# Performance work log

Measured on AMD Instinct MI355X. Metric: run time of the kernel, lower is better.

Reference implementation:

```python
import jax, jax.numpy as jnp
import numpy as np

N_NODES = 100000
N_EDGES = 1600000
FEAT = 64
HID = 128
HEADS = 4
OUT = 128
EPS_BN = 1e-5


def _gat_layer(h_in, src, dst, W, a_src, a_dst, bias, heads, out_c, concat, n_nodes):
    # h: [N, H, C]
    h = (h_in @ W).reshape(n_nodes, heads, out_c)
    alpha_src = jnp.sum(h * a_src, axis=-1)  # [N, H]
    alpha_dst = jnp.sum(h * a_dst, axis=-1)  # [N, H]
    e = jax.nn.leaky_relu(alpha_src[src] + alpha_dst[dst], negative_slope=0.2)  # [E, H]
    # segment softmax over incoming edges of each dst node
    e_max = jax.ops.segment_max(e, dst, num_segments=n_nodes)  # [N, H]
    ex = jnp.exp(e - e_max[dst])
    denom = jax.ops.segment_sum(ex, dst, num_segments=n_nodes)  # [N, H]
    alpha = ex / denom[dst]  # [E, H]
    # weighted scatter-aggregate of source features
    out = jax.ops.segment_sum(h[src] * alpha[:, :, None], dst, num_segments=n_nodes)  # [N, H, C]
    if concat:
        out = out.reshape(n_nodes, heads * out_c)
    else:
        out = out.mean(axis=1)
    return out + bias


def setup_inputs() -> dict:
    key = jax.random.key(0)
    ks = jax.random.split(key, 12)
    s = 0.1
    x = jax.random.normal(ks[0], (N_NODES, FEAT), dtype=jnp.float32)
    edge_index = jax.random.randint(ks[1], (2, N_EDGES), 0, N_NODES, dtype=jnp.int64)
    C1 = HID // HEADS
    return {
        "x": x,
        "edge_index": edge_index,
        "Wp": jax.random.normal(ks[2], (FEAT, HID), jnp.float32) * s,
        "bp": jnp.zeros((HID,), jnp.float32),
        "W1": jax.random.normal(ks[3], (HID, HEADS * C1), jnp.float32) * s,
        "att_src1": jax.random.normal(ks[4], (HEADS, C1), jnp.float32) * s,
        "att_dst1": jax.random.normal(ks[5], (HEADS, C1), jnp.float32) * s,
        "b1": jnp.zeros((HID,), jnp.float32),
        "gamma": jnp.ones((HID,), jnp.float32),
        "beta": jnp.zeros((HID,), jnp.float32),
        "W2": jax.random.normal(ks[6], (HID, HEADS * OUT), jnp.float32) * s,
        "att_src2": jax.random.normal(ks[7], (HEADS, OUT), jnp.float32) * s,
        "att_dst2": jax.random.normal(ks[8], (HEADS, OUT), jnp.float32) * s,
        "b2": jnp.zeros((OUT,), jnp.float32),
        "Wo": jax.random.normal(ks[9], (OUT, OUT), jnp.float32) * s,
        "bo": jnp.zeros((OUT,), jnp.float32),
    }


def reference(x, edge_index, Wp, bp, W1, att_src1, att_dst1, b1, gamma, beta,
              W2, att_src2, att_dst2, b2, Wo, bo):
    n = x.shape[0]
    # add self-loops (PyG GATConv default)
    loop = jnp.arange(n, dtype=edge_index.dtype)
    src = jnp.concatenate([edge_index[0], loop])
    dst = jnp.concatenate([edge_index[1], loop])

    h = jax.nn.relu(x @ Wp + bp)  # node_proj + relu

    # layer 1: concat heads -> HID
    h = _gat_layer(h, src, dst, W1, att_src1, att_dst1, b1, HEADS, HID // HEADS, True, n)
    # BatchNorm1d eval (fresh running stats: mean=0, var=1) + ELU (dropout off in eval)
    h = h * (gamma / jnp.sqrt(1.0 + EPS_BN)) + beta
    h = jax.nn.elu(h)

    # layer 2: average heads -> OUT
    h = _gat_layer(h, src, dst, W2, att_src2, att_dst2, b2, HEADS, OUT, False, n)

    # batch=None path: mean over all nodes
    g = h.mean(axis=0, keepdims=True)  # [1, OUT]
    return jax.nn.relu(g @ Wo + bo)
```

## Files before the change

### kernel.cpp

```cpp
#include <hip/hip_runtime.h>

#define N_N 100000
#define N_E 1600000
#define E_T (N_E + N_N)

#define NBKT 196
#define BKT_CAP 12288
#define CHUNK 4096
#define EPT 16

typedef long long ll;
typedef unsigned int uint;
typedef unsigned short ushort;
typedef unsigned char uchar;
typedef float floatx2 __attribute__((ext_vector_type(2)));

__device__ __forceinline__ float lrelu(float v){ return v > 0.f ? v : 0.2f*v; }

__device__ __forceinline__ uint pk_fp8_quad(float a, float b, float c, float d){
  int w = __builtin_amdgcn_cvt_pk_fp8_f32(a, b, 0, false);
  w = __builtin_amdgcn_cvt_pk_fp8_f32(c, d, w, true);
  return (uint)w;
}
__device__ __forceinline__ floatx2 unpk_fp8(uint v, int wsel){
  floatx2 lo = __builtin_amdgcn_cvt_pk_f32_fp8((int)v, false);
  floatx2 hi = __builtin_amdgcn_cvt_pk_f32_fp8((int)v, true);
  return wsel ? hi : lo;
}

__global__ void k_detect(const int* __restrict__ ei32, int* __restrict__ mode) {
  int m = 1;
  for (int i = 1; i < 16; i += 2) if (ei32[i] != 0) m = 0;
  *mode = m;
}

__device__ __forceinline__ void load_edge(const void* eiv, int mode, int e, int& s, int& d) {
  if (e < N_E) {
    if (mode) {
      const ll* p = (const ll*)eiv;
      s = (int)p[e]; d = (int)p[N_E + e];
    } else {
      const int* p = (const int*)eiv;
      s = p[e]; d = p[N_E + e];
    }
  } else { s = d = e - N_E; }
}

__global__ void k_zeroi(int* __restrict__ p, int n) {
  for (int i = blockIdx.x*blockDim.x + threadIdx.x; i < n; i += gridDim.x*blockDim.x)
    p[i] = 0;
}

__global__ __launch_bounds__(256) void k_bucket_blk(const void* __restrict__ eiv,
    const int* __restrict__ modep, int* __restrict__ bktpos, uint* __restrict__ stage)
{
  __shared__ int cnt[NBKT], base[NBKT], lrank[NBKT];
  int m = *modep;
  int t = threadIdx.x;
  int e0 = blockIdx.x * CHUNK;
  int nedge = E_T - e0; if (nedge > CHUNK) nedge = CHUNK;
  for (int i = t; i < NBKT; i += 256) { cnt[i] = 0; lrank[i] = 0; }
  __syncthreads();
  uint pk[EPT]; int bb[EPT];
  #pragma unroll
  for (int i = 0; i < EPT; ++i) {
    int idx = t + i*256;
    if (idx < nedge) {
      int e = e0 + idx, s, d;
      load_edge(eiv, m, e, s, d);
      bb[i] = d >> 9;
      pk[i] = ((uint)(d & 511) << 17) | (uint)s;
      atomicAdd(&cnt[bb[i]], 1);
    } else bb[i] = -1;
  }
  __syncthreads();
  for (int i = t; i < NBKT; i += 256)
    if (cnt[i] > 0) base[i] = atomicAdd(&bktpos[i*16], cnt[i]);
  __syncthreads();
  #pragma unroll
  for (int i = 0; i < EPT; ++i) {
    if (bb[i] >= 0) {
      int b = bb[i];
      int r = atomicAdd(&lrank[b], 1);
      int off = base[b] + r;
      if (off < BKT_CAP) stage[(size_t)b*BKT_CAP + off] = pk[i];
    }
  }
}

__global__ void k_bktscan(const int* __restrict__ bktpos, int* __restrict__ bktbase,
    int* __restrict__ rptrN)
{
  if (threadIdx.x == 0) {
    int run = 0;
    for (int b = 0; b < NBKT; ++b) { bktbase[b] = run; run += bktpos[b*16]; }
    *rptrN = run;
  }
}

__global__ __launch_bounds__(256) void k_bucket2(const int* __restrict__ bktpos,
    const int* __restrict__ bktbase, const uint* __restrict__ stage,
    int* __restrict__ csr_col, int* __restrict__ rptr)
{
  __shared__ int cntA[512], pA[512], pB[512], lpos[512];
  int b = blockIdx.x, t = threadIdx.x;
  int cnt = bktpos[b*16];
  if (cnt > BKT_CAP) cnt = BKT_CAP;
  int base = bktbase[b];
  const uint* st = stage + (size_t)b*BKT_CAP;
  for (int i = t; i < 512; i += 256) { cntA[i] = 0; lpos[i] = 0; }
  __syncthreads();
  for (int i = t; i < cnt; i += 256) atomicAdd(&cntA[st[i] >> 17], 1);
  __syncthreads();
  int* src = pA; int* dst = pB;
  for (int i = t; i < 512; i += 256) pA[i] = cntA[i];
  __syncthreads();
  for (int off = 1; off < 512; off <<= 1) {
    for (int i = t; i < 512; i += 256) {
      int v = src[i]; if (i >= off) v += src[i - off]; dst[i] = v;
    }
    __syncthreads();
    int* tmp = src; src = dst; dst = tmp;
  }
  int nb0 = b*512;
  for (int i = t; i < 512; i += 256) {
    int node = nb0 + i;
    if (node < N_N) rptr[node] = base + src[i] - cntA[i];
  }
  __syncthreads();
  for (int i = t; i < cnt; i += 256) {
    uint pk = st[i];
    int dlow = (int)(pk >> 17), s = (int)(pk & 0x1FFFFu);
    int r = atomicAdd(&lpos[dlow], 1);
    csr_col[base + (src[dlow] - cntA[dlow]) + r] = s;
  }
}

__global__ __launch_bounds__(256) void k_fused12(const float* __restrict__ x,
    const float* __restrict__ Wp, const float* __restrict__ bp,
    const float* __restrict__ W1, const float* __restrict__ avs,
    const float* __restrict__ avd, uchar* __restrict__ Hb8,
    float* __restrict__ as_o, float* __restrict__ ad_o)
{
  __shared__ float wl[64*128];
  __shared__ float h0s[32*132];
  __shared__ float xr[32*68];
  const int t = threadIdx.x;
  const int r0g = blockIdx.x * 32;
  const int tx = t & 31, ty = t >> 5;
  const int c0 = tx*4, r0 = ty*4;
  for (int i = t; i < 64*128; i += 256) wl[i] = Wp[i];
  for (int i = t; i < 32*64; i += 256) {
    int r = i >> 6, k = i & 63;
    xr[r*68 + k] = x[(size_t)(r0g + r)*64 + k];
  }
  __syncthreads();
  {
    float acc[4][4] = {};
    for (int k = 0; k < 64; ++k) {
      float4 wv = *(const float4*)&wl[k*128 + c0];
      float x0 = xr[(r0+0)*68+k], x1 = xr[(r0+1)*68+k];
      float x2 = xr[(r0+2)*68+k], x3 = xr[(r0+3)*68+k];
      acc[0][0] += x0*wv.x; acc[0][1] += x0*wv.y; acc[0][2] += x0*wv.z; acc[0][3] += x0*wv.w;
      acc[1][0] += x1*wv.x; acc[1][1] += x1*wv.y; acc[1][2] += x1*wv.z; acc[1][3] += x1*wv.w;
      acc[2][0] += x2*wv.x; acc[2][1] += x2*wv.y; acc[2][2] += x2*wv.z; acc[2][3] += x2*wv.w;
      acc[3][0] += x3*wv.x; acc[3][1] += x3*wv.y; acc[3][2] += x3*wv.z; acc[3][3] += x3*wv.w;
    }
    float4 bb = *(const float4*)&bp[c0];
    for (int i = 0; i < 4; ++i) {
      h0s[(r0+i)*132 + c0    ] = fmaxf(acc[i][0] + bb.x, 0.f);
      h0s[(r0+i)*132 + c0 + 1] = fmaxf(acc[i][1] + bb.y, 0.f);
      h0s[(r0+i)*132 + c0 + 2] = fmaxf(acc[i][2] + bb.z, 0.f);
      h0s[(r0+i)*132 + c0 + 3] = fmaxf(acc[i][3] + bb.w, 0.f);
    }
  }
  float acc[4][4] = {};
  for (int kc = 0; kc < 2; ++kc) {
    const int k0 = kc*64;
    __syncthreads();
    for (int i = t; i < 64*128; i += 256) wl[i] = W1[k0*128 + i];
    __syncthreads();
    for (int k = 0; k < 64; ++k) {
      float4 wv = *(const float4*)&wl[k*128 + c0];
      int kk = k0 + k;
      float x0 = h0s[(r0+0)*132+kk], x1 = h0s[(r0+1)*132+kk];
      float x2 = h0s[(r0+2)*132+kk], x3 = h0s[(r0+3)*132+kk];
      acc[0][0] += x0*wv.x; acc[0][1] += x0*wv.y; acc[0][2] += x0*wv.z; acc[0][3] += x0*wv.w;
      acc[1][0] += x1*wv.x; acc[1][1] += x1*wv.y; acc[1][2] += x1*wv.z; acc[1][3] += x1*wv.w;
      acc[2][0] += x2*wv.x; acc[2][1] += x2*wv.y; acc[2][2] += x2*wv.z; acc[2][3] += x2*wv.w;
      acc[3][0] += x3*wv.x; acc[3][1] += x3*wv.y; acc[3][2] += x3*wv.z; acc[3][3] += x3*wv.w;
    }
  }
  for (int i = 0; i < 4; ++i) {
    int r = r0g + r0 + i;
    ((uint*)&Hb8[(size_t)r*128])[tx] =
      pk_fp8_quad(acc[i][0], acc[i][1], acc[i][2], acc[i][3]);
  }
  float4 sa = *(const float4*)&avs[c0];
  float4 da = *(const float4*)&avd[c0];
  for (int i = 0; i < 4; ++i) {
    float vs = acc[i][0]*sa.x + acc[i][1]*sa.y + acc[i][2]*sa.z + acc[i][3]*sa.w;
    float vd = acc[i][0]*da.x + acc[i][1]*da.y + acc[i][2]*da.z + acc[i][3]*da.w;
    vs += __shfl_xor(vs, 1); vs += __shfl_xor(vs, 2); vs += __shfl_xor(vs, 4);
    vd += __shfl_xor(vd, 1); vd += __shfl_xor(vd, 2); vd += __shfl_xor(vd, 4);
    if ((tx & 7) == 0) {
      int r = r0g + r0 + i;
      as_o[r*4 + (tx >> 3)] = vs;
      ad_o[r*4 + (tx >> 3)] = vd;
    }
  }
}

__global__ void k_fold2(const float* __restrict__ W2,
    const float* __restrict__ att_s2, const float* __restrict__ att_d2,
    float* __restrict__ vs2, float* __restrict__ vd2)
{
  int t = threadIdx.x;
  int k = t & 127, hh = t >> 7;
  float accs = 0.f, accd = 0.f;
  for (int c = 0; c < 128; ++c) {
    float w = W2[(size_t)k*512 + hh*128 + c];
    accs += w * att_s2[hh*128 + c];
    accd += w * att_d2[hh*128 + c];
  }
  vs2[hh*128 + k] = accs;
  vd2[hh*128 + k] = accd;
}

__global__ __launch_bounds__(256) void k_agg1(const int* __restrict__ rptr,
    const int* __restrict__ csr_col, const uchar* __restrict__ Hb8,
    const float* __restrict__ as1, const float* __restrict__ ad1,
    const float* __restrict__ b1, const float* __restrict__ gamma,
    const float* __restrict__ beta, const float* __restrict__ vs2,
    const float* __restrict__ vd2, uchar* __restrict__ a1f8,
    float* __restrict__ as2, float* __restrict__ ad2)
{
  int wid = threadIdx.x >> 6, l = threadIdx.x & 63;
  int n = blockIdx.x*4 + wid;
  if (n >= N_N) return;
  int jm = l & 15, hm = l >> 4;
  const int wsel = l & 1, widx = l >> 1;
  const int wsrc = l & 48;
  float adm = ad1[n*4 + hm];
  int beg = rptr[n], end = rptr[n+1];
  float accx = 0.f, accy = 0.f, den = 0.f;
  for (int e0 = beg; e0 < end; e0 += 16) {
    int ne = end - e0; if (ne > 16) ne = 16;
    int sM = 0; float wM = 0.f;
    if (jm < ne) {
      sM = csr_col[e0 + jm];
      wM = __expf(lrelu(as1[sM*4 + hm] + adm));
    }
    den += wM;
    int j = 0;
    for (; j + 4 <= ne; j += 4) {
      int s0 = __shfl(sM, j),   s1 = __shfl(sM, j+1);
      int s2 = __shfl(sM, j+2), s3 = __shfl(sM, j+3);
      uint h0 = ((const uint*)&Hb8[(size_t)s0*128])[widx];
      uint h1 = ((const uint*)&Hb8[(size_t)s1*128])[widx];
      uint h2 = ((const uint*)&Hb8[(size_t)s2*128])[widx];
      uint h3 = ((const uint*)&Hb8[(size_t)s3*128])[widx];
      float w0 = __shfl(wM, wsrc + j),   w1 = __shfl(wM, wsrc + j+1);
      float w2 = __shfl(wM, wsrc + j+2), w3 = __shfl(wM, wsrc + j+3);
      floatx2 v0 = unpk_fp8(h0, wsel), v1 = unpk_fp8(h1, wsel);
      floatx2 v2 = unpk_fp8(h2, wsel), v3 = unpk_fp8(h3, wsel);
      accx += w0*v0.x + w1*v1.x + w2*v2.x + w3*v3.x;
      accy += w0*v0.y + w1*v1.y + w2*v2.y + w3*v3.y;
    }
    for (; j < ne; ++j) {
      int s = __shfl(sM, j);
      float w = __shfl(wM, wsrc + j);
      uint hv = ((const uint*)&Hb8[(size_t)s*128])[widx];
      floatx2 dv = unpk_fp8(hv, wsel);
      accx += w * dv.x;
      accy += w * dv.y;
    }
  }
  den += __shfl_xor(den, 1); den += __shfl_xor(den, 2);
  den += __shfl_xor(den, 4); den += __shfl_xor(den, 8);
  float inv = 1.f / den;
  int c = 2*l;
  const float sc = 0.9999950000374997f;
  float vx = (accx*inv + b1[c])   * (gamma[c]   * sc) + beta[c];
  float vy = (accy*inv + b1[c+1]) * (gamma[c+1] * sc) + beta[c+1];
  vx = vx > 0.f ? vx : __expf(vx) - 1.f;
  vy = vy > 0.f ? vy : __expf(vy) - 1.f;
  int pk = __builtin_amdgcn_cvt_pk_fp8_f32(vx, vy, 0, false);
  *(ushort*)&a1f8[(size_t)n*128 + c] = (ushort)pk;
  #pragma unroll
  for (int hh = 0; hh < 4; ++hh) {
    float2 wsv = *(const float2*)&vs2[hh*128 + c];
    float2 wdv = *(const float2*)&vd2[hh*128 + c];
    float ps = wsv.x*vx + wsv.y*vy;
    float pd = wdv.x*vx + wdv.y*vy;
    ps += __shfl_xor(ps, 1); ps += __shfl_xor(ps, 2); ps += __shfl_xor(ps, 4);
    ps += __shfl_xor(ps, 8); ps += __shfl_xor(ps, 16); ps += __shfl_xor(ps, 32);
    pd += __shfl_xor(pd, 1); pd += __shfl_xor(pd, 2); pd += __shfl_xor(pd, 4);
    pd += __shfl_xor(pd, 8); pd += __shfl_xor(pd, 16); pd += __shfl_xor(pd, 32);
    if (l == 0) { as2[n*4 + hh] = ps; ad2[n*4 + hh] = pd; }
  }
}

__global__ __launch_bounds__(512) void k_tail2(const int* __restrict__ rptr,
    const int* __restrict__ csr_col, const uchar* __restrict__ a1f8,
    const float* __restrict__ as2, const float* __restrict__ ad2,
    float* __restrict__ u)
{
  int wid = threadIdx.x >> 6, l = threadIdx.x & 63;
  int jm = l & 15, hm = l >> 4;
  int c0 = jm * 8;
  const int wsrc = l & 48;
  float acc[8] = {};
  for (int n = blockIdx.x*8 + wid; n < N_N; n += gridDim.x*8) {
    int beg = rptr[n], end = rptr[n+1];
    float adm = ad2[n*4 + hm];
    float accn[8] = {};
    float dsum = 0.f;
    for (int e0 = beg; e0 < end; e0 += 16) {
      int ne = end - e0; if (ne > 16) ne = 16;
      int sM = 0; float wM = 0.f;
      if (jm < ne) {
        sM = csr_col[e0 + jm];
        wM = __expf(lrelu(as2[sM*4 + hm] + adm));
      }
      dsum += wM;
      int j = 0;
      for (; j + 2 <= ne; j += 2) {
        int sa = __shfl(sM, j), sb = __shfl(sM, j+1);
        uint2 ha = *(const uint2*)&a1f8[(size_t)sa*128 + c0];
        uint2 hb = *(const uint2*)&a1f8[(size_t)sb*128 + c0];
        float wa = __shfl(wM, wsrc + j), wb = __shfl(wM, wsrc + j+1);
        floatx2 a0 = __builtin_amdgcn_cvt_pk_f32_fp8((int)ha.x, false);
        floatx2 a1 = __builtin_amdgcn_cvt_pk_f32_fp8((int)ha.x, true);
        floatx2 a2 = __builtin_amdgcn_cvt_pk_f32_fp8((int)ha.y, false);
        floatx2 a3 = __builtin_amdgcn_cvt_pk_f32_fp8((int)ha.y, true);
        floatx2 b0 = __builtin_amdgcn_cvt_pk_f32_fp8((int)hb.x, false);
        floatx2 b1v = __builtin_amdgcn_cvt_pk_f32_fp8((int)hb.x, true);
        floatx2 b2 = __builtin_amdgcn_cvt_pk_f32_fp8((int)hb.y, false);
        floatx2 b3 = __builtin_amdgcn_cvt_pk_f32_fp8((int)hb.y, true);
        accn[0] += wa*a0.x + wb*b0.x; accn[1] += wa*a0.y + wb*b0.y;
        accn[2] += wa*a1.x + wb*b1v.x; accn[3] += wa*a1.y + wb*b1v.y;
        accn[4] += wa*a2.x + wb*b2.x; accn[5] += wa*a2.y + wb*b2.y;
        accn[6] += wa*a3.x + wb*b3.x; accn[7] += wa*a3.y + wb*b3.y;
      }
      for (; j < ne; ++j) {
        int s = __shfl(sM, j);
        float w = __shfl(wM, wsrc + j);
        uint2 hv = *(const uint2*)&a1f8[(size_t)s*128 + c0];
        floatx2 d0 = __builtin_amdgcn_cvt_pk_f32_fp8((int)hv.x, false);
        floatx2 d1 = __builtin_amdgcn_cvt_pk_f32_fp8((int)hv.x, true);
        floatx2 d2 = __builtin_amdgcn_cvt_pk_f32_fp8((int)hv.y, false);
        floatx2 d3 = __builtin_amdgcn_cvt_pk_f32_fp8((int)hv.y, true);
        accn[0] += w * d0.x; accn[1] += w * d0.y;
        accn[2] += w * d1.x; accn[3] += w * d1.y;
        accn[4] += w * d2.x; accn[5] += w * d2.y;
        accn[6] += w * d3.x; accn[7] += w * d3.y;
      }
    }
    dsum += __shfl_xor(dsum, 1); dsum += __shfl_xor(dsum, 2);
    dsum += __shfl_xor(dsum, 4); dsum += __shfl_xor(dsum, 8);
    float inv = 1.f / dsum;
    #pragma unroll
    for (int c = 0; c < 8; ++c) acc[c] += accn[c] * inv;
  }
  __shared__ float us[8][512];
  #pragma unroll
  for (int c = 0; c < 8; ++c) us[wid][hm*128 + c0 + c] = acc[c];
  __syncthreads();
  for (int i = threadIdx.x; i < 512; i += 512) {
    float v = 0.f;
    #pragma unroll
    for (int w = 0; w < 8; ++w) v += us[w][i];
    atomicAdd(&u[i], v);
  }
}

__global__ void k_final2(const float* __restrict__ u, const float* __restrict__ W2,
    const float* __restrict__ b2, const float* __restrict__ Wo,
    const float* __restrict__ bo, float* __restrict__ outp)
{
  __shared__ float g[128];
  int t = threadIdx.x;
  float acc = 0.f;
  for (int h = 0; h < 4; ++h)
    for (int k = 0; k < 128; ++k)
      acc += u[h*128 + k] * W2[(size_t)k*512 + h*128 + t];
  g[t] = acc * (1.f / (4.f * N_N)) + b2[t];
  __syncthreads();
  float o = 0.f;
  for (int c = 0; c < 128; ++c) o += g[c] * Wo[c*128 + t];
  o += bo[t];
  outp[t] = o > 0.f ? o : 0.f;
}

extern "C" void kernel_launch(void* const* d_in, const int* in_sizes, int n_in,
                              void* d_out, int out_size, void* d_ws, size_t ws_size,
                              hipStream_t stream) {
  const float* x    = (const float*)d_in[0];
  const void*  ei   = d_in[1];
  const float* Wp   = (const float*)d_in[2];
  const float* bp   = (const float*)d_in[3];
  const float* W1   = (const float*)d_in[4];
  const float* at_s1= (const float*)d_in[5];
  const float* at_d1= (const float*)d_in[6];
  const float* b1   = (const float*)d_in[7];
  const float* gamma= (const float*)d_in[8];
  const float* beta = (const float*)d_in[9];
  const float* W2   = (const float*)d_in[10];
  const float* at_s2= (const float*)d_in[11];
  const float* at_d2= (const float*)d_in[12];
  const float* b2   = (const float*)d_in[13];
  const float* Wo   = (const float*)d_in[14];
  const float* bo   = (const float*)d_in[15];

  const size_t NN = N_N;
  uchar* hb8   = (uchar*)d_ws;
  uchar* a1f8  = hb8 + NN*128;
  int*   csr_col = (int*)(a1f8 + NN*128);
  int*   rptr    = csr_col + E_T;
  uint*  stage   = (uint*)(rptr + N_N + 1);
  int*   bktpos  = (int*)(stage + (size_t)NBKT*BKT_CAP);
  int*   bktbase = bktpos + NBKT*16;
  float* as1     = (float*)(bktbase + NBKT);
  float* ad1     = as1 + NN*4;
  float* as2     = ad1 + NN*4;
  float* ad2     = as2 + NN*4;
  float* vs2     = ad2 + NN*4;
  float* vd2     = vs2 + 512;
  float* u       = vd2 + 512;
  int*   modep   = (int*)(u + 512);

  size_t required = ((char*)(modep + 1)) - (char*)d_ws;
  if (ws_size < required) return;

  const int NB4 = (N_N + 3) / 4;
  const int NCHUNK = (E_T + CHUNK - 1) / CHUNK;

  k_detect<<<1, 1, 0, stream>>>((const int*)ei, modep);
  k_zeroi<<<16, 256, 0, stream>>>(bktpos, NBKT*16);
  k_zeroi<<<2, 256, 0, stream>>>((int*)u, 512);
  k_bucket_blk<<<NCHUNK, 256, 0, stream>>>(ei, modep, bktpos, stage);
  k_bktscan<<<1, 64, 0, stream>>>(bktpos, bktbase, rptr + N_N);
  k_bucket2<<<NBKT, 256, 0, stream>>>(bktpos, bktbase, stage, csr_col, rptr);

  k_fused12<<<N_N/32, 256, 0, stream>>>(x, Wp, bp, W1, at_s1, at_d1, hb8, as1, ad1);
  k_fold2<<<1, 512, 0, stream>>>(W2, at_s2, at_d2, vs2, vd2);
  k_agg1<<<NB4, 256, 0, stream>>>(rptr, csr_col, hb8, as1, ad1, b1, gamma, beta,
                                  vs2, vd2, a1f8, as2, ad2);

  k_tail2<<<1024, 512, 0, stream>>>(rptr, csr_col, a1f8, as2, ad2, u);
  k_final2<<<1, 128, 0, stream>>>(u, W2, b2, Wo, bo, (float*)d_out);
}
```

Baseline: 387.0 us.

## Merge independent preprocessing kernels into one launch and use packed float2 accumulation

Folds mode detection and the two zeroing kernels into a single init kernel. Merges the edge bucketing, the node projection/layer-1 GEMM and the W2 attention fold into one heterogeneous kernel that dispatches on block index, so these independent stages run concurrently and no longer serialize across launches. The aggregation loops in agg1 and tail2 now accumulate in floatx2 vectors so the compiler can emit packed FMA instructions. Unifying the shared memory footprint may reduce occupancy for the bucketing blocks.

```diff
diff --git a/kernel.cpp b/kernel.cpp
--- a/kernel.cpp
+++ b/kernel.cpp
@@ -8,6 +8,7 @@
 #define BKT_CAP 12288
 #define CHUNK 4096
 #define EPT 16
+#define NPROJ (N_N/32)
 
 typedef long long ll;
 typedef unsigned int uint;
@@ -26,12 +27,6 @@
   floatx2 lo = __builtin_amdgcn_cvt_pk_f32_fp8((int)v, false);
   floatx2 hi = __builtin_amdgcn_cvt_pk_f32_fp8((int)v, true);
   return wsel ? hi : lo;
-}
-
-__global__ void k_detect(const int* __restrict__ ei32, int* __restrict__ mode) {
-  int m = 1;
-  for (int i = 1; i < 16; i += 2) if (ei32[i] != 0) m = 0;
-  *mode = m;
 }
 
 __device__ __forceinline__ void load_edge(const void* eiv, int mode, int e, int& s, int& d) {
@@ -46,45 +41,151 @@
   } else { s = d = e - N_E; }
 }
 
-__global__ void k_zeroi(int* __restrict__ p, int n) {
-  for (int i = blockIdx.x*blockDim.x + threadIdx.x; i < n; i += gridDim.x*blockDim.x)
-    p[i] = 0;
-}
-
-__global__ __launch_bounds__(256) void k_bucket_blk(const void* __restrict__ eiv,
-    const int* __restrict__ modep, int* __restrict__ bktpos, uint* __restrict__ stage)
-{
-  __shared__ int cnt[NBKT], base[NBKT], lrank[NBKT];
-  int m = *modep;
-  int t = threadIdx.x;
-  int e0 = blockIdx.x * CHUNK;
-  int nedge = E_T - e0; if (nedge > CHUNK) nedge = CHUNK;
-  for (int i = t; i < NBKT; i += 256) { cnt[i] = 0; lrank[i] = 0; }
-  __syncthreads();
-  uint pk[EPT]; int bb[EPT];
-  #pragma unroll
-  for (int i = 0; i < EPT; ++i) {
-    int idx = t + i*256;
-    if (idx < nedge) {
-      int e = e0 + idx, s, d;
-      load_edge(eiv, m, e, s, d);
-      bb[i] = d >> 9;
-      pk[i] = ((uint)(d & 511) << 17) | (uint)s;
-      atomicAdd(&cnt[bb[i]], 1);
-    } else bb[i] = -1;
-  }
-  __syncthreads();
-  for (int i = t; i < NBKT; i += 256)
-    if (cnt[i] > 0) base[i] = atomicAdd(&bktpos[i*16], cnt[i]);
-  __syncthreads();
-  #pragma unroll
-  for (int i = 0; i < EPT; ++i) {
-    if (bb[i] >= 0) {
-      int b = bb[i];
-      int r = atomicAdd(&lrank[b], 1);
-      int off = base[b] + r;
-      if (off < BKT_CAP) stage[(size_t)b*BKT_CAP + off] = pk[i];
-    }
+__global__ __launch_bounds__(256) void k_init(const int* __restrict__ ei32,
+    int* __restrict__ bktpos, int* __restrict__ u512, int* __restrict__ mode)
+{
+  int i = blockIdx.x*256 + threadIdx.x;
+  if (i < NBKT*16) bktpos[i] = 0;
+  if (i < 512) u512[i] = 0;
+  if (i == 0) {
+    int m = 1;
+    for (int k = 1; k < 16; k += 2) if (ei32[k] != 0) m = 0;
+    *mode = m;
+  }
+}
+
+__global__ __launch_bounds__(256) void k_mega(
+    const void* __restrict__ eiv, const int* __restrict__ modep,
+    int* __restrict__ bktpos, uint* __restrict__ stage,
+    const float* __restrict__ x, const float* __restrict__ Wp,
+    const float* __restrict__ bp, const float* __restrict__ W1,
+    const float* __restrict__ avs, const float* __restrict__ avd,
+    uchar* __restrict__ Hb8, float* __restrict__ as_o, float* __restrict__ ad_o,
+    const float* __restrict__ W2, const float* __restrict__ att_s2,
+    const float* __restrict__ att_d2, float* __restrict__ vs2, float* __restrict__ vd2)
+{
+  __shared__ float smem[8192 + 4224 + 2176];
+  const int blk = blockIdx.x;
+  const int t = threadIdx.x;
+  const int NCH = (E_T + CHUNK - 1) / CHUNK;
+
+  if (blk < NCH) {
+    int* cnt   = (int*)smem;
+    int* base  = cnt + NBKT;
+    int* lrank = base + NBKT;
+    int m = *modep;
+    int e0 = blk * CHUNK;
+    int nedge = E_T - e0; if (nedge > CHUNK) nedge = CHUNK;
+    for (int i = t; i < NBKT; i += 256) { cnt[i] = 0; lrank[i] = 0; }
+    __syncthreads();
+    uint pk[EPT]; int bb[EPT];
+    #pragma unroll
+    for (int i = 0; i < EPT; ++i) {
+      int idx = t + i*256;
+      if (idx < nedge) {
+        int e = e0 + idx, s, d;
+        load_edge(eiv, m, e, s, d);
+        bb[i] = d >> 9;
+        pk[i] = ((uint)(d & 511) << 17) | (uint)s;
+        atomicAdd(&cnt[bb[i]], 1);
+      } else bb[i] = -1;
+    }
+    __syncthreads();
+    for (int i = t; i < NBKT; i += 256)
+      if (cnt[i] > 0) base[i] = atomicAdd(&bktpos[i*16], cnt[i]);
+    __syncthreads();
+    #pragma unroll
+    for (int i = 0; i < EPT; ++i) {
+      if (bb[i] >= 0) {
+        int b = bb[i];
+        int r = atomicAdd(&lrank[b], 1);
+        int off = base[b] + r;
+        if (off < BKT_CAP) stage[(size_t)b*BKT_CAP + off] = pk[i];
+      }
+    }
+    return;
+  }
+
+  if (blk < NCH + NPROJ) {
+    float* wl  = smem;
+    float* h0s = smem + 8192;
+    float* xr  = smem + 8192 + 4224;
+    const int r0g = (blk - NCH) * 32;
+    const int tx = t & 31, ty = t >> 5;
+    const int c0 = tx*4, r0 = ty*4;
+    for (int i = t; i < 64*128; i += 256) wl[i] = Wp[i];
+    for (int i = t; i < 32*64; i += 256) {
+      int r = i >> 6, k = i & 63;
+      xr[r*68 + k] = x[(size_t)(r0g + r)*64 + k];
+    }
+    __syncthreads();
+    {
+      float acc[4][4] = {};
+      for (int k = 0; k < 64; ++k) {
+        float4 wv = *(const float4*)&wl[k*128 + c0];
+        float x0 = xr[(r0+0)*68+k], x1 = xr[(r0+1)*68+k];
+        float x2 = xr[(r0+2)*68+k], x3 = xr[(r0+3)*68+k];
+        acc[0][0] += x0*wv.x; acc[0][1] += x0*wv.y; acc[0][2] += x0*wv.z; acc[0][3] += x0*wv.w;
+        acc[1][0] += x1*wv.x; acc[1][1] += x1*wv.y; acc[1][2] += x1*wv.z; acc[1][3] += x1*wv.w;
+        acc[2][0] += x2*wv.x; acc[2][1] += x2*wv.y; acc[2][2] += x2*wv.z; acc[2][3] += x2*wv.w;
+        acc[3][0] += x3*wv.x; acc[3][1] += x3*wv.y; acc[3][2] += x3*wv.z; acc[3][3] += x3*wv.w;
+      }
+      float4 bb = *(const float4*)&bp[c0];
+      for (int i = 0; i < 4; ++i) {
+        h0s[(r0+i)*132 + c0    ] = fmaxf(acc[i][0] + bb.x, 0.f);
+        h0s[(r0+i)*132 + c0 + 1] = fmaxf(acc[i][1] + bb.y, 0.f);
+        h0s[(r0+i)*132 + c0 + 2] = fmaxf(acc[i][2] + bb.z, 0.f);
+        h0s[(r0+i)*132 + c0 + 3] = fmaxf(acc[i][3] + bb.w, 0.f);
+      }
+    }
+    float acc[4][4] = {};
+    for (int kc = 0; kc < 2; ++kc) {
+      const int k0 = kc*64;
+      __syncthreads();
+      for (int i = t; i < 64*128; i += 256) wl[i] = W1[k0*128 + i];
+      __syncthreads();
+      for (int k = 0; k < 64; ++k) {
+        float4 wv = *(const float4*)&wl[k*128 + c0];
+        int kk = k0 + k;
+        float x0 = h0s[(r0+0)*132+kk], x1 = h0s[(r0+1)*132+kk];
+        float x2 = h0s[(r0+2)*132+kk], x3 = h0s[(r0+3)*132+kk];
+        acc[0][0] += x0*wv.x; acc[0][1] += x0*wv.y; acc[0][2] += x0*wv.z; acc[0][3] += x0*wv.w;
+        acc[1][0] += x1*wv.x; acc[1][1] += x1*wv.y; acc[1][2] += x1*wv.z; acc[1][3] += x1*wv.w;
+        acc[2][0] += x2*wv.x; acc[2][1] += x2*wv.y; acc[2][2] += x2*wv.z; acc[2][3] += x2*wv.w;
+        acc[3][0] += x3*wv.x; acc[3][1] += x3*wv.y; acc[3][2] += x3*wv.z; acc[3][3] += x3*wv.w;
+      }
+    }
+    for (int i = 0; i < 4; ++i) {
+      int r = r0g + r0 + i;
+      ((uint*)&Hb8[(size_t)r*128])[tx] =
+        pk_fp8_quad(acc[i][0], acc[i][1], acc[i][2], acc[i][3]);
+    }
+    float4 sa = *(const float4*)&avs[c0];
+    float4 da = *(const float4*)&avd[c0];
+    for (int i = 0; i < 4; ++i) {
+      float vs = acc[i][0]*sa.x + acc[i][1]*sa.y + acc[i][2]*sa.z + acc[i][3]*sa.w;
+      float vd = acc[i][0]*da.x + acc[i][1]*da.y + acc[i][2]*da.z + acc[i][3]*da.w;
+      vs += __shfl_xor(vs, 1); vs += __shfl_xor(vs, 2); vs += __shfl_xor(vs, 4);
+      vd += __shfl_xor(vd, 1); vd += __shfl_xor(vd, 2); vd += __shfl_xor(vd, 4);
+      if ((tx & 7) == 0) {
+        int r = r0g + r0 + i;
+        as_o[r*4 + (tx >> 3)] = vs;
+        ad_o[r*4 + (tx >> 3)] = vd;
+      }
+    }
+    return;
+  }
+
+  for (int t2 = t; t2 < 512; t2 += 256) {
+    int k = t2 & 127, hh = t2 >> 7;
+    float accs = 0.f, accd = 0.f;
+    for (int c = 0; c < 128; ++c) {
+      float w = W2[(size_t)k*512 + hh*128 + c];
+      accs += w * att_s2[hh*128 + c];
+      accd += w * att_d2[hh*128 + c];
+    }
+    vs2[hh*128 + k] = accs;
+    vd2[hh*128 + k] = accd;
   }
 }
 
@@ -134,97 +235,6 @@
     int r = atomicAdd(&lpos[dlow], 1);
     csr_col[base + (src[dlow] - cntA[dlow]) + r] = s;
   }
-}
-
-__global__ __launch_bounds__(256) void k_fused12(const float* __restrict__ x,
-    const float* __restrict__ Wp, const float* __restrict__ bp,
-    const float* __restrict__ W1, const float* __restrict__ avs,
-    const float* __restrict__ avd, uchar* __restrict__ Hb8,
-    float* __restrict__ as_o, float* __restrict__ ad_o)
-{
-  __shared__ float wl[64*128];
-  __shared__ float h0s[32*132];
-  __shared__ float xr[32*68];
-  const int t = threadIdx.x;
-  const int r0g = blockIdx.x * 32;
-  const int tx = t & 31, ty = t >> 5;
-  const int c0 = tx*4, r0 = ty*4;
-  for (int i = t; i < 64*128; i += 256) wl[i] = Wp[i];
-  for (int i = t; i < 32*64; i += 256) {
-    int r = i >> 6, k = i & 63;
-    xr[r*68 + k] = x[(size_t)(r0g + r)*64 + k];
-  }
-  __syncthreads();
-  {
-    float acc[4][4] = {};
-    for (int k = 0; k < 64; ++k) {
-      float4 wv = *(const float4*)&wl[k*128 + c0];
-      float x0 = xr[(r0+0)*68+k], x1 = xr[(r0+1)*68+k];
-      float x2 = xr[(r0+2)*68+k], x3 = xr[(r0+3)*68+k];
-      acc[0][0] += x0*wv.x; acc[0][1] += x0*wv.y; acc[0][2] += x0*wv.z; acc[0][3] += x0*wv.w;
-      acc[1][0] += x1*wv.x; acc[1][1] += x1*wv.y; acc[1][2] += x1*wv.z; acc[1][3] += x1*wv.w;
-      acc[2][0] += x2*wv.x; acc[2][1] += x2*wv.y; acc[2][2] += x2*wv.z; acc[2][3] += x2*wv.w;
-      acc[3][0] += x3*wv.x; acc[3][1] += x3*wv.y; acc[3][2] += x3*wv.z; acc[3][3] += x3*wv.w;
-    }
-    float4 bb = *(const float4*)&bp[c0];
-    for (int i = 0; i < 4; ++i) {
-      h0s[(r0+i)*132 + c0    ] = fmaxf(acc[i][0] + bb.x, 0.f);
-      h0s[(r0+i)*132 + c0 + 1] = fmaxf(acc[i][1] + bb.y, 0.f);
-      h0s[(r0+i)*132 + c0 + 2] = fmaxf(acc[i][2] + bb.z, 0.f);
-      h0s[(r0+i)*132 + c0 + 3] = fmaxf(acc[i][3] + bb.w, 0.f);
-    }
-  }
-  float acc[4][4] = {};
-  for (int kc = 0; kc < 2; ++kc) {
-    const int k0 = kc*64;
-    __syncthreads();
-    for (int i = t; i < 64*128; i += 256) wl[i] = W1[k0*128 + i];
-    __syncthreads();
-    for (int k = 0; k < 64; ++k) {
-      float4 wv = *(const float4*)&wl[k*128 + c0];
-      int kk = k0 + k;
-      float x0 = h0s[(r0+0)*132+kk], x1 = h0s[(r0+1)*132+kk];
-      float x2 = h0s[(r0+2)*132+kk], x3 = h0s[(r0+3)*132+kk];
-      acc[0][0] += x0*wv.x; acc[0][1] += x0*wv.y; acc[0][2] += x0*wv.z; acc[0][3] += x0*wv.w;
-      acc[1][0] += x1*wv.x; acc[1][1] += x1*wv.y; acc[1][2] += x1*wv.z; acc[1][3] += x1*wv.w;
-      acc[2][0] += x2*wv.x; acc[2][1] += x2*wv.y; acc[2][2] += x2*wv.z; acc[2][3] += x2*wv.w;
-      acc[3][0] += x3*wv.x; acc[3][1] += x3*wv.y; acc[3][2] += x3*wv.z; acc[3][3] += x3*wv.w;
-    }
-  }
-  for (int i = 0; i < 4; ++i) {
-    int r = r0g + r0 + i;
-    ((uint*)&Hb8[(size_t)r*128])[tx] =
-      pk_fp8_quad(acc[i][0], acc[i][1], acc[i][2], acc[i][3]);
-  }
-  float4 sa = *(const float4*)&avs[c0];
-  float4 da = *(const float4*)&avd[c0];
-  for (int i = 0; i < 4; ++i) {
-    float vs = acc[i][0]*sa.x + acc[i][1]*sa.y + acc[i][2]*sa.z + acc[i][3]*sa.w;
-    float vd = acc[i][0]*da.x + acc[i][1]*da.y + acc[i][2]*da.z + acc[i][3]*da.w;
-    vs += __shfl_xor(vs, 1); vs += __shfl_xor(vs, 2); vs += __shfl_xor(vs, 4);
-    vd += __shfl_xor(vd, 1); vd += __shfl_xor(vd, 2); vd += __shfl_xor(vd, 4);
-    if ((tx & 7) == 0) {
-      int r = r0g + r0 + i;
-      as_o[r*4 + (tx >> 3)] = vs;
-      ad_o[r*4 + (tx >> 3)] = vd;
-    }
-  }
-}
-
-__global__ void k_fold2(const float* __restrict__ W2,
-    const float* __restrict__ att_s2, const float* __restrict__ att_d2,
-    float* __restrict__ vs2, float* __restrict__ vd2)
-{
-  int t = threadIdx.x;
-  int k = t & 127, hh = t >> 7;
-  float accs = 0.f, accd = 0.f;
-  for (int c = 0; c < 128; ++c) {
-    float w = W2[(size_t)k*512 + hh*128 + c];
-    accs += w * att_s2[hh*128 + c];
-    accd += w * att_d2[hh*128 + c];
-  }
-  vs2[hh*128 + k] = accs;
-  vd2[hh*128 + k] = accd;
 }
 
 __global__ __launch_bounds__(256) void k_agg1(const int* __restrict__ rptr,
@@ -243,7 +253,8 @@
   const int wsrc = l & 48;
   float adm = ad1[n*4 + hm];
   int beg = rptr[n], end = rptr[n+1];
-  float accx = 0.f, accy = 0.f, den = 0.f;
+  floatx2 acc2 = {0.f, 0.f};
+  float den = 0.f;
   for (int e0 = beg; e0 < end; e0 += 16) {
     int ne = end - e0; if (ne > 16) ne = 16;
     int sM = 0; float wM = 0.f;
@@ -264,16 +275,16 @@
       float w2 = __shfl(wM, wsrc + j+2), w3 = __shfl(wM, wsrc + j+3);
       floatx2 v0 = unpk_fp8(h0, wsel), v1 = unpk_fp8(h1, wsel);
       floatx2 v2 = unpk_fp8(h2, wsel), v3 = unpk_fp8(h3, wsel);
-      accx += w0*v0.x + w1*v1.x + w2*v2.x + w3*v3.x;
-      accy += w0*v0.y + w1*v1.y + w2*v2.y + w3*v3.y;
+      floatx2 W0 = {w0, w0}, W1v = {w1, w1}, W2v = {w2, w2}, W3 = {w3, w3};
+      acc2 += W0*v0 + W1v*v1 + W2v*v2 + W3*v3;
     }
     for (; j < ne; ++j) {
       int s = __shfl(sM, j);
       float w = __shfl(wM, wsrc + j);
       uint hv = ((const uint*)&Hb8[(size_t)s*128])[widx];
       floatx2 dv = unpk_fp8(hv, wsel);
-      accx += w * dv.x;
-      accy += w * dv.y;
+      floatx2 W = {w, w};
+      acc2 += W*dv;
     }
   }
   den += __shfl_xor(den, 1); den += __shfl_xor(den, 2);
@@ -281,8 +292,8 @@
   float inv = 1.f / den;
   int c = 2*l;
   const float sc = 0.9999950000374997f;
-  float vx = (accx*inv + b1[c])   * (gamma[c]   * sc) + beta[c];
-  float vy = (accy*inv + b1[c+1]) * (gamma[c+1] * sc) + beta[c+1];
+  float vx = (acc2.x*inv + b1[c])   * (gamma[c]   * sc) + beta[c];
+  float vy = (acc2.y*inv + b1[c+1]) * (gamma[c+1] * sc) + beta[c+1];
   vx = vx > 0.f ? vx : __expf(vx) - 1.f;
   vy = vy > 0.f ? vy : __expf(vy) - 1.f;
   int pk = __builtin_amdgcn_cvt_pk_fp8_f32(vx, vy, 0, false);
@@ -310,11 +321,11 @@
   int jm = l & 15, hm = l >> 4;
   int c0 = jm * 8;
   const int wsrc = l & 48;
-  float acc[8] = {};
+  floatx2 acc[4] = {};
   for (int n = blockIdx.x*8 + wid; n < N_N; n += gridDim.x*8) {
     int beg = rptr[n], end = rptr[n+1];
     float adm = ad2[n*4 + hm];
-    float accn[8] = {};
+    floatx2 an[4] = {};
     float dsum = 0.f;
     for (int e0 = beg; e0 < end; e0 += 16) {
       int ne = end - e0; if (ne > 16) ne = 16;
@@ -330,42 +341,40 @@
         uint2 ha = *(const uint2*)&a1f8[(size_t)sa*128 + c0];
         uint2 hb = *(const uint2*)&a1f8[(size_t)sb*128 + c0];
         float wa = __shfl(wM, wsrc + j), wb = __shfl(wM, wsrc + j+1);
-        floatx2 a0 = __builtin_amdgcn_cvt_pk_f32_fp8((int)ha.x, false);
-        floatx2 a1 = __builtin_amdgcn_cvt_pk_f32_fp8((int)ha.x, true);
-        floatx2 a2 = __builtin_amdgcn_cvt_pk_f32_fp8((int)ha.y, false);
-        floatx2 a3 = __builtin_amdgcn_cvt_pk_f32_fp8((int)ha.y, true);
-        floatx2 b0 = __builtin_amdgcn_cvt_pk_f32_fp8((int)hb.x, false);
-        floatx2 b1v = __builtin_amdgcn_cvt_pk_f32_fp8((int)hb.x, true);
-        floatx2 b2 = __builtin_amdgcn_cvt_pk_f32_fp8((int)hb.y, false);
-        floatx2 b3 = __builtin_amdgcn_cvt_pk_f32_fp8((int)hb.y, true);
-        accn[0] += wa*a0.x + wb*b0.x; accn[1] += wa*a0.y + wb*b0.y;
-        accn[2] += wa*a1.x + wb*b1v.x; accn[3] += wa*a1.y + wb*b1v.y;
-        accn[4] += wa*a2.x + wb*b2.x; accn[5] += wa*a2.y + wb*b2.y;
-        accn[6] += wa*a3.x + wb*b3.x; accn[7] += wa*a3.y + wb*b3.y;
+        floatx2 WA = {wa, wa}, WB = {wb, wb};
+        an[0] += WA*__builtin_amdgcn_cvt_pk_f32_fp8((int)ha.x, false)
+               + WB*__builtin_amdgcn_cvt_pk_f32_fp8((int)hb.x, false);
+        an[1] += WA*__builtin_amdgcn_cvt_pk_f32_fp8((int)ha.x, true)
+               + WB*__builtin_amdgcn_cvt_pk_f32_fp8((int)hb.x, true);
+        an[2] += WA*__builtin_amdgcn_cvt_pk_f32_fp8((int)ha.y, false)
+               + WB*__builtin_amdgcn_cvt_pk_f32_fp8((int)hb.y, false);
+        an[3] += WA*__builtin_amdgcn_cvt_pk_f32_fp8((int)ha.y, true)
+               + WB*__builtin_amdgcn_cvt_pk_f32_fp8((int)hb.y, true);
       }
       for (; j < ne; ++j) {
         int s = __shfl(sM, j);
         float w = __shfl(wM, wsrc + j);
         uint2 hv = *(const uint2*)&a1f8[(size_t)s*128 + c0];
-        floatx2 d0 = __builtin_amdgcn_cvt_pk_f32_fp8((int)hv.x, false);
-        floatx2 d1 = __builtin_amdgcn_cvt_pk_f32_fp8((int)hv.x, true);
-        floatx2 d2 = __builtin_amdgcn_cvt_pk_f32_fp8((int)hv.y, false);
-        floatx2 d3 = __builtin_amdgcn_cvt_pk_f32_fp8((int)hv.y, true);
-        accn[0] += w * d0.x; accn[1] += w * d0.y;
-        accn[2] += w * d1.x; accn[3] += w * d1.y;
-        accn[4] += w * d2.x; accn[5] += w * d2.y;
-        accn[6] += w * d3.x; accn[7] += w * d3.y;
+        floatx2 W = {w, w};
+        an[0] += W*__builtin_amdgcn_cvt_pk_f32_fp8((int)hv.x, false);
+        an[1] += W*__builtin_amdgcn_cvt_pk_f32_fp8((int)hv.x, true);
+        an[2] += W*__builtin_amdgcn_cvt_pk_f32_fp8((int)hv.y, false);
+        an[3] += W*__builtin_amdgcn_cvt_pk_f32_fp8((int)hv.y, true);
       }
     }
     dsum += __shfl_xor(dsum, 1); dsum += __shfl_xor(dsum, 2);
     dsum += __shfl_xor(dsum, 4); dsum += __shfl_xor(dsum, 8);
     float inv = 1.f / dsum;
+    floatx2 IV = {inv, inv};
     #pragma unroll
-    for (int c = 0; c < 8; ++c) acc[c] += accn[c] * inv;
+    for (int c = 0; c < 4; ++c) acc[c] += an[c] * IV;
   }
   __shared__ float us[8][512];
   #pragma unroll
-  for (int c = 0; c < 8; ++c) us[wid][hm*128 + c0 + c] = acc[c];
+  for (int c = 0; c < 4; ++c) {
+    us[wid][hm*128 + c0 + 2*c    ] = acc[c].x;
+    us[wid][hm*128 + c0 + 2*c + 1] = acc[c].y;
+  }
   __syncthreads();
   for (int i = threadIdx.x; i < 512; i += 512) {
     float v = 0.f;
@@ -436,18 +445,15 @@
   const int NB4 = (N_N + 3) / 4;
   const int NCHUNK = (E_T + CHUNK - 1) / CHUNK;
 
-  k_detect<<<1, 1, 0, stream>>>((const int*)ei, modep);
-  k_zeroi<<<16, 256, 0, stream>>>(bktpos, NBKT*16);
-  k_zeroi<<<2, 256, 0, stream>>>((int*)u, 512);
-  k_bucket_blk<<<NCHUNK, 256, 0, stream>>>(ei, modep, bktpos, stage);
+  k_init<<<17, 256, 0, stream>>>((const int*)ei, bktpos, (int*)u, modep);
+  k_mega<<<NCHUNK + NPROJ + 1, 256, 0, stream>>>(
+      ei, modep, bktpos, stage,
+      x, Wp, bp, W1, at_s1, at_d1, hb8, as1, ad1,
+      W2, at_s2, at_d2, vs2, vd2);
   k_bktscan<<<1, 64, 0, stream>>>(bktpos, bktbase, rptr + N_N);
   k_bucket2<<<NBKT, 256, 0, stream>>>(bktpos, bktbase, stage, csr_col, rptr);
-
-  k_fused12<<<N_N/32, 256, 0, stream>>>(x, Wp, bp, W1, at_s1, at_d1, hb8, as1, ad1);
-  k_fold2<<<1, 512, 0, stream>>>(W2, at_s2, at_d2, vs2, vd2);
   k_agg1<<<NB4, 256, 0, stream>>>(rptr, csr_col, hb8, as1, ad1, b1, gamma, beta,
                                   vs2, vd2, a1f8, as2, ad2);
-
   k_tail2<<<1024, 512, 0, stream>>>(rptr, csr_col, a1f8, as2, ad2, u);
   k_final2<<<1, 128, 0, stream>>>(u, W2, b2, Wo, bo, (float*)d_out);
 }
```

Measured after the change: 360.8 us. 1.07x faster.
